# Optimization experiments

Hardware: AMD Instinct MI355X
Metric: run time of the kernel (lower is better)

## Reference

```python
import jax, jax.numpy as jnp
import numpy as np

MUL = 32          # channel multiplicity of node features (32x0e + 32x1o)
N_SPEC = 4        # one-hot species dim (node_attrs = 4x0e)
N_EMB = 8         # radial (bessel) embedding dim
HID = 8           # invariant_neurons
TP_W = 4 * MUL    # tp.weight_numel: 4 'uvu' paths, 32 weights each
INV_SQRT3 = 0.5773502691896258


def setup_inputs() -> dict:
    key = jax.random.key(0)
    ks = jax.random.split(key, 13)
    N, E = 50000, 800000
    node_features = jax.random.normal(ks[0], (N, 4 * MUL), jnp.float32)
    node_attrs = jax.random.uniform(ks[1], (N, N_SPEC), dtype=jnp.float32)
    edge_index = jax.random.randint(ks[2], (2, E), 0, N)
    edge_attrs = jax.random.normal(ks[3], (E, 4), jnp.float32)          # SH: [0e | 1o(3)]
    edge_embedding = jax.random.uniform(ks[4], (E, N_EMB), dtype=jnp.float32)
    # learned parameters
    W1_s = jax.random.normal(ks[5], (MUL, MUL), jnp.float32)            # linear_1 scalar block
    W1_v = jax.random.normal(ks[6], (MUL, MUL), jnp.float32)            # linear_1 vector block
    fc_w1 = jax.random.normal(ks[7], (N_EMB, HID), jnp.float32)         # radial MLP layer 1
    fc_w2 = jax.random.normal(ks[8], (HID, TP_W), jnp.float32)          # radial MLP -> tp weights
    W2_s = jax.random.normal(ks[9], (2 * MUL, MUL), jnp.float32)        # linear_2: 64x0e -> 32x0e
    W2_v = jax.random.normal(ks[10], (2 * MUL, MUL), jnp.float32)       # linear_2: 64x1o -> 32x1o
    Wsc_s = jax.random.normal(ks[11], (MUL, N_SPEC, MUL), jnp.float32)  # sc: 0e x 0e -> 0e (uvw)
    Wsc_v = jax.random.normal(ks[12], (MUL, N_SPEC, MUL), jnp.float32)  # sc: 1o x 0e -> 1o (uvw)
    return dict(node_features=node_features, node_attrs=node_attrs,
                edge_attrs=edge_attrs, edge_embedding=edge_embedding,
                W1_s=W1_s, W1_v=W1_v, fc_w1=fc_w1, fc_w2=fc_w2,
                W2_s=W2_s, W2_v=W2_v, Wsc_s=Wsc_s, Wsc_v=Wsc_v,
                edge_index=edge_index)


def reference(node_features, node_attrs, edge_attrs, edge_embedding,
              W1_s, W1_v, fc_w1, fc_w2, W2_s, W2_v, Wsc_s, Wsc_v, edge_index):
    N = node_features.shape[0]
    edge_src = edge_index[1]
    edge_dst = edge_index[0]

    # split node features into scalar (32x0e) and vector (32x1o) blocks
    s = node_features[:, :MUL]                       # [N, 32]
    v = node_features[:, MUL:].reshape(N, MUL, 3)    # [N, 32, 3]

    # --- self-connection: FullyConnectedTensorProduct(features, node_attrs) ---
    sc_norm = 1.0 / jnp.sqrt(jnp.float32(MUL * N_SPEC))
    sc_s = jnp.einsum('nu,na,uaw->nw', s, node_attrs, Wsc_s) * sc_norm
    sc_v = jnp.einsum('nui,na,uaw->nwi', v, node_attrs, Wsc_v) * sc_norm

    # --- linear_1 (per-irrep linear, fan-in normalized) ---
    l1 = 1.0 / jnp.sqrt(jnp.float32(MUL))
    s1 = (s @ W1_s) * l1                                   # [N, 32]
    v1 = jnp.einsum('nui,uw->nwi', v, W1_v) * l1           # [N, 32, 3]

    # --- radial MLP: edge_embedding -> per-edge tp weights (silu) ---
    h = jax.nn.silu((edge_embedding @ fc_w1) / jnp.sqrt(jnp.float32(N_EMB)))
    w = (h @ fc_w2) / jnp.sqrt(jnp.float32(HID))           # [E, 128]
    w0, w1, w2, w3 = w[:, :MUL], w[:, MUL:2*MUL], w[:, 2*MUL:3*MUL], w[:, 3*MUL:]

    # --- gather source-node features per edge ---
    ss = s1[edge_src]                                      # [E, 32]
    vv = v1[edge_src]                                      # [E, 32, 3]
    a0 = edge_attrs[:, 0]                                  # [E]    0e SH
    a1 = edge_attrs[:, 1:4]                                # [E, 3] 1o SH

    # --- 'uvu' CG tensor product (4 paths) with per-edge weights ---
    o_s0 = w0 * ss * a0[:, None]                                    # 0e x 0e -> 0e
    o_s1 = w3 * jnp.einsum('eui,ei->eu', vv, a1) * INV_SQRT3        # 1o x 1o -> 0e
    o_v0 = w1[:, :, None] * ss[:, :, None] * a1[:, None, :]        # 0e x 1o -> 1o
    o_v1 = w2[:, :, None] * vv * a0[:, None, None]                 # 1o x 0e -> 1o

    eS = jnp.concatenate([o_s0, o_s1], axis=1)             # [E, 64] (64x0e)
    eV = jnp.concatenate([o_v0, o_v1], axis=1)             # [E, 64, 3] (64x1o)

    # --- scatter-add to destination nodes ---
    S = jax.ops.segment_sum(eS, edge_dst, num_segments=N)  # [N, 64]
    V = jax.ops.segment_sum(eV, edge_dst, num_segments=N)  # [N, 64, 3]

    # --- linear_2 (64x0e+64x1o -> 32x0e+32x1o) ---
    l2 = 1.0 / jnp.sqrt(jnp.float32(2 * MUL))
    s_out = (S @ W2_s) * l2
    v_out = jnp.einsum('nui,uw->nwi', V, W2_v) * l2

    # --- residual self-connection ---
    s_out = s_out + sc_s
    v_out = v_out + sc_v
    return jnp.concatenate([s_out, v_out.reshape(N, MUL * 3)], axis=1)  # [N, 128]
```

## Files before the change

kernel.cpp:

```cpp
#include <hip/hip_runtime.h>
#include <math.h>


typedef float  v2f __attribute__((ext_vector_type(2)));
typedef float  v4f __attribute__((ext_vector_type(4)));

__device__ __forceinline__ unsigned short f2bf(float x) {
    unsigned u = __float_as_uint(x);
    u += 0x7FFFu + ((u >> 16) & 1u);
    return (unsigned short)(u >> 16);
}
__device__ __forceinline__ float bf2f(unsigned short h) {
    return __uint_as_float(((unsigned)h) << 16);
}

__global__ __launch_bounds__(256) void node_prep(
    const float* __restrict__ nf, const float* __restrict__ W1_s,
    const float* __restrict__ W1_v, const int* __restrict__ eidx,
    int* __restrict__ cnt, ushort* __restrict__ sv1, int N, int E)
{
    __shared__ float w1s[1024];
    __shared__ float w1v[1024];
    __shared__ float nrow[8][128];

    for (long long e = (long long)blockIdx.x * 256 + threadIdx.x; e < E;
         e += (long long)gridDim.x * 256)
        atomicAdd(cnt + eidx[(int)e], 1);

    int g = threadIdx.x >> 5;
    int w = threadIdx.x & 31;
    int n = blockIdx.x * 8 + g;

    for (int i = threadIdx.x; i < 1024; i += 256) {
        w1s[i] = W1_s[i];
        w1v[i] = W1_v[i];
    }
    if (n < N) {
        float4 q = *(const float4*)(nf + (size_t)n * 128 + w * 4);
        *(float4*)&nrow[g][w * 4] = q;
    }
    __syncthreads();
    if (n >= N) return;

    const float l1 = 0.17677669529663687f;
    const float* r = nrow[g];
    float ss = 0.f, vx = 0.f, vy = 0.f, vz = 0.f;
#pragma unroll 8
    for (int u = 0; u < 32; ++u) {
        float ws = w1s[u * 32 + w];
        float wv = w1v[u * 32 + w];
        ss += r[u] * ws;
        vx += r[32 + u * 3 + 0] * wv;
        vy += r[32 + u * 3 + 1] * wv;
        vz += r[32 + u * 3 + 2] * wv;
    }
    ushort4 o;
    o.x = f2bf(ss * l1); o.y = f2bf(vx * l1);
    o.z = f2bf(vy * l1); o.w = f2bf(vz * l1);
    *(ushort4*)(sv1 + (size_t)n * 128 + w * 4) = o;
}


__global__ __launch_bounds__(1024) void scan_a(
    const int* __restrict__ cnt, int* __restrict__ rs,
    int* __restrict__ bsum, int N)
{
    int i = blockIdx.x * 1024 + threadIdx.x;
    int lane = threadIdx.x & 63;
    int wid = threadIdx.x >> 6;
    int v = (i < N) ? cnt[i] : 0;
    int incl = v;
#pragma unroll
    for (int d = 1; d < 64; d <<= 1) {
        int t = __shfl_up(incl, d);
        if (lane >= d) incl += t;
    }
    __shared__ int wtot[16];
    __shared__ int woff[16];
    if (lane == 63) wtot[wid] = incl;
    __syncthreads();
    if (wid == 0) {
        int t = (lane < 16) ? wtot[lane] : 0;
        int s = t;
#pragma unroll
        for (int d = 1; d < 16; d <<= 1) {
            int q = __shfl_up(s, d);
            if (lane >= d) s += q;
        }
        if (lane < 16) woff[lane] = s - t;
        if (lane == 15) bsum[blockIdx.x] = s;
    }
    __syncthreads();
    if (i < N) rs[i] = woff[wid] + incl - v;
}

__global__ __launch_bounds__(64) void scan_b(
    const int* __restrict__ bsum, int* __restrict__ boff, int nb)
{
    int lane = threadIdx.x;
    int carry = 0;
    for (int base = 0; base < nb; base += 64) {
        int i = base + lane;
        int v = (i < nb) ? bsum[i] : 0;
        int s = v;
#pragma unroll
        for (int d = 1; d < 64; d <<= 1) {
            int t = __shfl_up(s, d);
            if (lane >= d) s += t;
        }
        if (i < nb) boff[i] = carry + s - v;
        carry += __shfl(s, 63);
    }
}

__global__ __launch_bounds__(256) void scatter_kernel(
    const int* __restrict__ eidx, int* __restrict__ rs,
    const int* __restrict__ boff, int* __restrict__ perm, int E)
{
    int e = blockIdx.x * 256 + threadIdx.x;
    if (e < E) {
        int d = eidx[e];
        int p = atomicAdd(rs + d, 1) + boff[d >> 10];
        perm[p] = e;
    }
}


__global__ __launch_bounds__(64) void reduce_kernel(
    const float* __restrict__ ea, const float* __restrict__ ee,
    const float* __restrict__ fc1, const float* __restrict__ fc2,
    const ushort* __restrict__ sv1, const int* __restrict__ eidx,
    const int* __restrict__ perm, const int* __restrict__ rs_end,
    const int* __restrict__ boff, const int* __restrict__ cnt,
    float* __restrict__ SV, int N, int E)
{
    __shared__ float rec[64][20];

    int l = threadIdx.x;
    int h = l >> 5;
    int u = l & 31;
    int n = blockIdx.x;

    const float rs8 = 0.35355339059327373f;
    const float inv_sqrt3 = 0.5773502691896258f;

    v2f f01[8], f23[8];
#pragma unroll
    for (int k = 0; k < 8; ++k) {
        f01[k].x = fc2[k * 128 + u];
        f01[k].y = fc2[k * 128 + 32 + u];
        f23[k].x = fc2[k * 128 + 64 + u];
        f23[k].y = fc2[k * 128 + 96 + u];
    }

    int count = cnt[n];
    int start = rs_end[n] + boff[n >> 10] - count;

    float aS0 = 0.f, aS1 = 0.f;
    float aV0x = 0.f, aV0y = 0.f, aV0z = 0.f;
    float aV1x = 0.f, aV1y = 0.f, aV1z = 0.f;

    for (int j0 = 0; j0 < count; j0 += 64) {
        int nk = count - j0; if (nk > 64) nk = 64;
        if (l < nk) {
            int e = perm[start + j0 + l];
            const float* eep = ee + (size_t)e * 8;
            v4f e0 = *(const v4f*)eep;
            v4f e1 = *(const v4f*)(eep + 4);
            float ev[8] = {e0.x, e0.y, e0.z, e0.w, e1.x, e1.y, e1.z, e1.w};
            float hh[8];
#pragma unroll
            for (int k = 0; k < 8; ++k) {
                float t = 0.f;
#pragma unroll
                for (int i = 0; i < 8; ++i) t += ev[i] * fc1[i * 8 + k];
                t *= rs8;
                hh[k] = t * __builtin_amdgcn_rcpf(1.f + __expf(-t)) * rs8;
            }
            float* rr = &rec[l][0];
            *(v4f*)rr       = (v4f){hh[0], hh[1], hh[2], hh[3]};
            *(v4f*)(rr + 4) = (v4f){hh[4], hh[5], hh[6], hh[7]};
            *(v4f*)(rr + 8) = *(const v4f*)(ea + (size_t)e * 4);
            rr[12] = __int_as_float(eidx[E + e]);
        }
        int pairs = (nk + 1) >> 1;
        int last = nk - 1;
        int s0 = __float_as_int(rec[h <= last ? h : last][12]);
        ushort4 q = *(const ushort4*)(sv1 + (size_t)s0 * 128 + u * 4);
        for (int jj = 0; jj < pairs; ++jj) {
            int slot = jj * 2 + h;
            int nslot = slot + 2 <= last ? slot + 2 : last;
            int sN = __float_as_int(rec[nslot][12]);
            ushort4 qn = *(const ushort4*)(sv1 + (size_t)sN * 128 + u * 4);

            float msk = (slot <= last) ? 1.f : 0.f;
            int slotc = slot <= last ? slot : last;
            const float* rr = &rec[slotc][0];
            v4f H0 = *(const v4f*)rr;
            v4f H1 = *(const v4f*)(rr + 4);
            v4f A  = *(const v4f*)(rr + 8);
            float ss = bf2f(q.x) * msk;
            float vx = bf2f(q.y), vy = bf2f(q.z), vz = bf2f(q.w);

            v2f w01 = H0.x * f01[0] + H0.y * f01[1] + H0.z * f01[2] + H0.w * f01[3]
                    + H1.x * f01[4] + H1.y * f01[5] + H1.z * f01[6] + H1.w * f01[7];
            v2f w23 = H0.x * f23[0] + H0.y * f23[1] + H0.z * f23[2] + H0.w * f23[3]
                    + H1.x * f23[4] + H1.y * f23[5] + H1.z * f23[6] + H1.w * f23[7];

            float dv = (vx * A.y + vy * A.z + vz * A.w) * msk;
            aS0 += w01.x * (ss * A.x);
            aS1 += w23.y * dv;
            float c1 = w01.y * ss;
            aV0x += c1 * A.y; aV0y += c1 * A.z; aV0z += c1 * A.w;
            float c2 = w23.x * A.x * msk;
            aV1x += c2 * vx; aV1y += c2 * vy; aV1z += c2 * vz;
            q = qn;
        }
    }

    aS0  += __shfl_xor(aS0, 32);
    aS1  += __shfl_xor(aS1, 32);
    aV0x += __shfl_xor(aV0x, 32);
    aV0y += __shfl_xor(aV0y, 32);
    aV0z += __shfl_xor(aV0z, 32);
    aV1x += __shfl_xor(aV1x, 32);
    aV1y += __shfl_xor(aV1y, 32);
    aV1z += __shfl_xor(aV1z, 32);

    if (h == 0) {
        float* o = SV + (size_t)n * 256 + u * 8;
        *(v4f*)o       = (v4f){aS0, aS1 * inv_sqrt3, aV0x, aV0y};
        *(v4f*)(o + 4) = (v4f){aV0z, aV1x, aV1y, aV1z};
    }
}


__global__ __launch_bounds__(256) void edge_kernel(
    const float* __restrict__ ea, const float* __restrict__ ee,
    const float* __restrict__ fc1, const float* __restrict__ fc2,
    const ushort* __restrict__ sv1, const int* __restrict__ eidx,
    float* __restrict__ SV, int E)
{
    long long tid = (long long)blockIdx.x * 256 + threadIdx.x;
    int e = (int)(tid >> 5);
    int u = (int)(tid & 31);
    if (e >= E) return;
    const float rs8 = 0.35355339059327373f;
    const float inv_sqrt3 = 0.5773502691896258f;
    float ev[8];
#pragma unroll
    for (int i = 0; i < 8; ++i) ev[i] = ee[(size_t)e * 8 + i];
    float h[8];
#pragma unroll
    for (int k = 0; k < 8; ++k) {
        float t = 0.f;
#pragma unroll
        for (int i = 0; i < 8; ++i) t += ev[i] * fc1[i * 8 + k];
        t *= rs8;
        h[k] = t / (1.f + expf(-t));
    }
    float w0 = 0.f, w1 = 0.f, w2 = 0.f, w3 = 0.f;
#pragma unroll
    for (int k = 0; k < 8; ++k) {
        const float* f2 = fc2 + k * 128;
        float hk = h[k];
        w0 += hk * f2[u];
        w1 += hk * f2[32 + u];
        w2 += hk * f2[64 + u];
        w3 += hk * f2[96 + u];
    }
    w0 *= rs8; w1 *= rs8; w2 *= rs8; w3 *= rs8;
    int dst = eidx[e];
    int src = eidx[E + e];
    float a0 = ea[(size_t)e * 4 + 0];
    float ax = ea[(size_t)e * 4 + 1];
    float ay = ea[(size_t)e * 4 + 2];
    float az = ea[(size_t)e * 4 + 3];
    ushort4 q = *(const ushort4*)(sv1 + (size_t)src * 128 + u * 4);
    float ss = bf2f(q.x), vx = bf2f(q.y), vy = bf2f(q.z), vz = bf2f(q.w);
    float dv = vx * ax + vy * ay + vz * az;
    float* o = SV + (size_t)dst * 256 + u * 8;
    atomicAdd(o + 0, w0 * ss * a0);
    atomicAdd(o + 1, w3 * dv * inv_sqrt3);
    float c1 = w1 * ss;
    atomicAdd(o + 2, c1 * ax);
    atomicAdd(o + 3, c1 * ay);
    atomicAdd(o + 4, c1 * az);
    float c2 = w2 * a0;
    atomicAdd(o + 5, c2 * vx);
    atomicAdd(o + 6, c2 * vy);
    atomicAdd(o + 7, c2 * vz);
}


__global__ __launch_bounds__(256) void node_final(
    const float* __restrict__ SV, const float* __restrict__ W2_s,
    const float* __restrict__ W2_v, const float* __restrict__ nf,
    const float* __restrict__ nattr, const float* __restrict__ Wsc_s,
    const float* __restrict__ Wsc_v, float* __restrict__ out, int N)
{
    __shared__ float wq[4096];
    __shared__ float wsp[4096];
    __shared__ float wvp[4096];
    __shared__ float svt[8][8][32];
    __shared__ float nrow[8][128];

    int g = threadIdx.x >> 5;
    int w = threadIdx.x & 31;

    for (int i = threadIdx.x; i < 1024; i += 256) {
        int uu = i >> 5, ww = i & 31;
        *(float4*)&wq[i * 4] = make_float4(W2_s[i], W2_s[i + 1024],
                                           W2_v[i], W2_v[i + 1024]);
        const float* ps = Wsc_s + (size_t)uu * 128 + ww;
        const float* pv = Wsc_v + (size_t)uu * 128 + ww;
        *(float4*)&wsp[i * 4] = make_float4(ps[0], ps[32], ps[64], ps[96]);
        *(float4*)&wvp[i * 4] = make_float4(pv[0], pv[32], pv[64], pv[96]);
    }
    __syncthreads();

    const float l2 = 0.125f;
    const float sc_norm = 0.08838834764831843f;

    for (int t = 0; t < 4; ++t) {
        int n = blockIdx.x * 32 + g * 4 + t;
        if (n >= N) continue;
        const float* svp = SV + (size_t)n * 256 + w * 8;
        float4 p0 = *(const float4*)svp;
        float4 p1 = *(const float4*)(svp + 4);
        svt[g][0][w] = p0.x; svt[g][1][w] = p0.y;
        svt[g][2][w] = p0.z; svt[g][3][w] = p0.w;
        svt[g][4][w] = p1.x; svt[g][5][w] = p1.y;
        svt[g][6][w] = p1.z; svt[g][7][w] = p1.w;
        float4 q = *(const float4*)(nf + (size_t)n * 128 + w * 4);
        *(float4*)&nrow[g][w * 4] = q;
        float at0 = nattr[(size_t)n * 4 + 0];
        float at1 = nattr[(size_t)n * 4 + 1];
        float at2 = nattr[(size_t)n * 4 + 2];
        float at3 = nattr[(size_t)n * 4 + 3];

        float sa = 0.f, va0 = 0.f, va1 = 0.f, va2 = 0.f;
        float scs = 0.f, scv0 = 0.f, scv1 = 0.f, scv2 = 0.f;
#pragma unroll
        for (int u = 0; u < 32; ++u) {
            float4 qw = *(const float4*)&wq[(u * 32 + w) * 4];
            sa  += svt[g][0][u] * qw.x + svt[g][1][u] * qw.y;
            va0 += svt[g][2][u] * qw.z + svt[g][5][u] * qw.w;
            va1 += svt[g][3][u] * qw.z + svt[g][6][u] * qw.w;
            va2 += svt[g][4][u] * qw.z + svt[g][7][u] * qw.w;
            float4 ps = *(const float4*)&wsp[(u * 32 + w) * 4];
            float4 pv = *(const float4*)&wvp[(u * 32 + w) * 4];
            float cs = at0 * ps.x + at1 * ps.y + at2 * ps.z + at3 * ps.w;
            float cv = at0 * pv.x + at1 * pv.y + at2 * pv.z + at3 * pv.w;
            scs  += nrow[g][u] * cs;
            scv0 += nrow[g][32 + u * 3 + 0] * cv;
            scv1 += nrow[g][32 + u * 3 + 1] * cv;
            scv2 += nrow[g][32 + u * 3 + 2] * cv;
        }
        float* orow = out + (size_t)n * 128;
        orow[w] = sa * l2 + scs * sc_norm;
        orow[32 + w * 3 + 0] = va0 * l2 + scv0 * sc_norm;
        orow[32 + w * 3 + 1] = va1 * l2 + scv1 * sc_norm;
        orow[32 + w * 3 + 2] = va2 * l2 + scv2 * sc_norm;
    }
}

extern "C" void kernel_launch(void* const* d_in, const int* in_sizes, int n_in,
                              void* d_out, int out_size, void* d_ws, size_t ws_size,
                              hipStream_t stream) {
    const float* nf    = (const float*)d_in[0];
    const float* nattr = (const float*)d_in[1];
    const float* ea    = (const float*)d_in[2];
    const float* ee    = (const float*)d_in[3];
    const float* W1_s  = (const float*)d_in[4];
    const float* W1_v  = (const float*)d_in[5];
    const float* fc1   = (const float*)d_in[6];
    const float* fc2   = (const float*)d_in[7];
    const float* W2_s  = (const float*)d_in[8];
    const float* W2_v  = (const float*)d_in[9];
    const float* Wsc_s = (const float*)d_in[10];
    const float* Wsc_v = (const float*)d_in[11];
    const int*   eidx  = (const int*)d_in[12];

    int N = in_sizes[0] / 128;
    int E = in_sizes[12] / 2;

    float* ws = (float*)d_ws;
    ushort* sv1 = (ushort*)ws;
    float* SV  = ws + (size_t)N * 64;
    int* cnt  = (int*)(SV + (size_t)N * 256);
    int* rs   = cnt + N;
    int* bsum = rs + N;
    int* boff = bsum + 64;
    int* perm = boff + 64;

    size_t needed = ((size_t)N * 320 + 2 * (size_t)N + 128 + (size_t)E) * 4;

    int nb_node = (N + 7) / 8;
    int nbE = (E + 255) / 256;
    int nb_final = (N + 31) / 32;

    if (ws_size >= needed) {
        hipMemsetAsync(cnt, 0, (size_t)N * sizeof(int), stream);
        node_prep<<<nb_node, 256, 0, stream>>>(nf, W1_s, W1_v, eidx, cnt, sv1, N, E);
        int nbS = (N + 1023) / 1024;
        scan_a<<<nbS, 1024, 0, stream>>>(cnt, rs, bsum, N);
        scan_b<<<1, 64, 0, stream>>>(bsum, boff, nbS);
        scatter_kernel<<<nbE, 256, 0, stream>>>(eidx, rs, boff, perm, E);
        reduce_kernel<<<N, 64, 0, stream>>>(ea, ee, fc1, fc2, sv1, eidx,
                                            perm, rs, boff, cnt, SV, N, E);
        node_final<<<nb_final, 256, 0, stream>>>(SV, W2_s, W2_v, nf, nattr,
                                                 Wsc_s, Wsc_v, (float*)d_out, N);
    } else {
        hipMemsetAsync(SV, 0, (size_t)N * 256 * sizeof(float), stream);
        node_prep<<<nb_node, 256, 0, stream>>>(nf, W1_s, W1_v, eidx, cnt, sv1, N, E);
        long long tot = (long long)E * 32;
        int nb_edge = (int)((tot + 255) / 256);
        edge_kernel<<<nb_edge, 256, 0, stream>>>(ea, ee, fc1, fc2, sv1, eidx, SV, E);
        node_final<<<nb_final, 256, 0, stream>>>(SV, W2_s, W2_v, nf, nattr,
                                                 Wsc_s, Wsc_v, (float*)d_out, N);
    }
}
```

Measured before the change: 251.8 us.

## Precompute radial MLP in scatter pass into sorted bf16 edge buffers

The scatter kernel now evaluates the radial MLP hidden layer per edge and writes the hidden values, edge attributes (both bf16) and source index directly into destination-sorted buffers. The reduce kernel no longer does random gathers through a permutation array or recomputes the MLP, and it reads contiguous records instead. The reduce kernel also packs two nodes per 128-thread block, and the intermediate SV buffer is stored in bf16 and read by a new node_final variant. This cuts gather traffic and SV bandwidth at the cost of extra bf16 rounding of hidden activations, edge attributes and aggregates.

```diff
diff --git a/kernel.cpp b/kernel.cpp
--- a/kernel.cpp
+++ b/kernel.cpp
@@ -13,6 +13,15 @@
 __device__ __forceinline__ float bf2f(unsigned short h) {
     return __uint_as_float(((unsigned)h) << 16);
 }
+__device__ __forceinline__ unsigned pack_bf(float lo, float hi) {
+    unsigned ul = __float_as_uint(lo);
+    ul = (ul + (0x7FFFu + ((ul >> 16) & 1u))) >> 16;
+    unsigned uh = __float_as_uint(hi);
+    uh = (uh + (0x7FFFu + ((uh >> 16) & 1u))) & 0xFFFF0000u;
+    return ul | uh;
+}
+__device__ __forceinline__ float bf_lo(unsigned p) { return __uint_as_float(p << 16); }
+__device__ __forceinline__ float bf_hi(unsigned p) { return __uint_as_float(p & 0xFFFF0000u); }
 
 __global__ __launch_bounds__(256) void node_prep(
     const float* __restrict__ nf, const float* __restrict__ W1_s,
@@ -113,35 +122,64 @@
     }
 }
 
-__global__ __launch_bounds__(256) void scatter_kernel(
-    const int* __restrict__ eidx, int* __restrict__ rs,
-    const int* __restrict__ boff, int* __restrict__ perm, int E)
+__global__ __launch_bounds__(256) void scatter_build(
+    const float* __restrict__ ea, const float* __restrict__ ee,
+    const float* __restrict__ fc1, const int* __restrict__ eidx,
+    int* __restrict__ rs, const int* __restrict__ boff,
+    ushort* __restrict__ hb, ushort* __restrict__ ab,
+    int* __restrict__ srcb, int E)
 {
     int e = blockIdx.x * 256 + threadIdx.x;
-    if (e < E) {
-        int d = eidx[e];
-        int p = atomicAdd(rs + d, 1) + boff[d >> 10];
-        perm[p] = e;
-    }
-}
-
-
-__global__ __launch_bounds__(64) void reduce_kernel(
-    const float* __restrict__ ea, const float* __restrict__ ee,
-    const float* __restrict__ fc1, const float* __restrict__ fc2,
-    const ushort* __restrict__ sv1, const int* __restrict__ eidx,
-    const int* __restrict__ perm, const int* __restrict__ rs_end,
+    if (e >= E) return;
+    const float rs8 = 0.35355339059327373f;
+
+    int d = eidx[e];
+    int p = atomicAdd(rs + d, 1) + boff[d >> 10];
+
+    const float* eep = ee + (size_t)e * 8;
+    v4f e0 = *(const v4f*)eep;
+    v4f e1 = *(const v4f*)(eep + 4);
+    float ev[8] = {e0.x, e0.y, e0.z, e0.w, e1.x, e1.y, e1.z, e1.w};
+    float hh[8];
+#pragma unroll
+    for (int k = 0; k < 8; ++k) {
+        float t = 0.f;
+#pragma unroll
+        for (int i = 0; i < 8; ++i) t += ev[i] * fc1[i * 8 + k];
+        t *= rs8;
+        hh[k] = t * __builtin_amdgcn_rcpf(1.f + __expf(-t)) * rs8;
+    }
+    uint4 hp;
+    hp.x = pack_bf(hh[0], hh[1]);
+    hp.y = pack_bf(hh[2], hh[3]);
+    hp.z = pack_bf(hh[4], hh[5]);
+    hp.w = pack_bf(hh[6], hh[7]);
+    *(uint4*)(hb + (size_t)p * 8) = hp;
+    v4f a = *(const v4f*)(ea + (size_t)e * 4);
+    uint2 ap;
+    ap.x = pack_bf(a.x, a.y);
+    ap.y = pack_bf(a.z, a.w);
+    *(uint2*)(ab + (size_t)p * 4) = ap;
+    srcb[p] = eidx[E + e];
+}
+
+
+__global__ __launch_bounds__(128) void reduce_kernel(
+    const float* __restrict__ fc2, const ushort* __restrict__ sv1,
+    const ushort* __restrict__ hb, const ushort* __restrict__ ab,
+    const int* __restrict__ srcb, const int* __restrict__ rs_end,
     const int* __restrict__ boff, const int* __restrict__ cnt,
-    float* __restrict__ SV, int N, int E)
-{
-    __shared__ float rec[64][20];
-
-    int l = threadIdx.x;
-    int h = l >> 5;
-    int u = l & 31;
-    int n = blockIdx.x;
-
-    const float rs8 = 0.35355339059327373f;
+    ushort* __restrict__ SVb, int N)
+{
+    __shared__ float rec[2][64][20];
+
+    int wv = threadIdx.x >> 6;
+    int l  = threadIdx.x & 63;
+    int h  = l >> 5;
+    int u  = l & 31;
+    int n = blockIdx.x * 2 + wv;
+    if (n >= N) return;
+
     const float inv_sqrt3 = 0.5773502691896258f;
 
     v2f f01[8], f23[8];
@@ -163,39 +201,29 @@
     for (int j0 = 0; j0 < count; j0 += 64) {
         int nk = count - j0; if (nk > 64) nk = 64;
         if (l < nk) {
-            int e = perm[start + j0 + l];
-            const float* eep = ee + (size_t)e * 8;
-            v4f e0 = *(const v4f*)eep;
-            v4f e1 = *(const v4f*)(eep + 4);
-            float ev[8] = {e0.x, e0.y, e0.z, e0.w, e1.x, e1.y, e1.z, e1.w};
-            float hh[8];
-#pragma unroll
-            for (int k = 0; k < 8; ++k) {
-                float t = 0.f;
-#pragma unroll
-                for (int i = 0; i < 8; ++i) t += ev[i] * fc1[i * 8 + k];
-                t *= rs8;
-                hh[k] = t * __builtin_amdgcn_rcpf(1.f + __expf(-t)) * rs8;
-            }
-            float* rr = &rec[l][0];
-            *(v4f*)rr       = (v4f){hh[0], hh[1], hh[2], hh[3]};
-            *(v4f*)(rr + 4) = (v4f){hh[4], hh[5], hh[6], hh[7]};
-            *(v4f*)(rr + 8) = *(const v4f*)(ea + (size_t)e * 4);
-            rr[12] = __int_as_float(eidx[E + e]);
+            size_t idx = (size_t)(start + j0 + l);
+            uint4 hq = *(const uint4*)(hb + idx * 8);
+            uint2 aq = *(const uint2*)(ab + idx * 4);
+            int s = srcb[idx];
+            float* rr = &rec[wv][l][0];
+            *(v4f*)rr       = (v4f){bf_lo(hq.x), bf_hi(hq.x), bf_lo(hq.y), bf_hi(hq.y)};
+            *(v4f*)(rr + 4) = (v4f){bf_lo(hq.z), bf_hi(hq.z), bf_lo(hq.w), bf_hi(hq.w)};
+            *(v4f*)(rr + 8) = (v4f){bf_lo(aq.x), bf_hi(aq.x), bf_lo(aq.y), bf_hi(aq.y)};
+            rr[12] = __int_as_float(s);
         }
         int pairs = (nk + 1) >> 1;
         int last = nk - 1;
-        int s0 = __float_as_int(rec[h <= last ? h : last][12]);
+        int s0 = __float_as_int(rec[wv][h <= last ? h : last][12]);
         ushort4 q = *(const ushort4*)(sv1 + (size_t)s0 * 128 + u * 4);
         for (int jj = 0; jj < pairs; ++jj) {
             int slot = jj * 2 + h;
             int nslot = slot + 2 <= last ? slot + 2 : last;
-            int sN = __float_as_int(rec[nslot][12]);
+            int sN = __float_as_int(rec[wv][nslot][12]);
             ushort4 qn = *(const ushort4*)(sv1 + (size_t)sN * 128 + u * 4);
 
             float msk = (slot <= last) ? 1.f : 0.f;
             int slotc = slot <= last ? slot : last;
-            const float* rr = &rec[slotc][0];
+            const float* rr = &rec[wv][slotc][0];
             v4f H0 = *(const v4f*)rr;
             v4f H1 = *(const v4f*)(rr + 4);
             v4f A  = *(const v4f*)(rr + 8);
@@ -228,9 +256,83 @@
     aV1z += __shfl_xor(aV1z, 32);
 
     if (h == 0) {
-        float* o = SV + (size_t)n * 256 + u * 8;
-        *(v4f*)o       = (v4f){aS0, aS1 * inv_sqrt3, aV0x, aV0y};
-        *(v4f*)(o + 4) = (v4f){aV0z, aV1x, aV1y, aV1z};
+        uint4 o;
+        o.x = pack_bf(aS0, aS1 * inv_sqrt3);
+        o.y = pack_bf(aV0x, aV0y);
+        o.z = pack_bf(aV0z, aV1x);
+        o.w = pack_bf(aV1y, aV1z);
+        *(uint4*)(SVb + (size_t)n * 256 + u * 8) = o;
+    }
+}
+
+
+__global__ __launch_bounds__(256) void node_final(
+    const ushort* __restrict__ SVb, const float* __restrict__ W2_s,
+    const float* __restrict__ W2_v, const float* __restrict__ nf,
+    const float* __restrict__ nattr, const float* __restrict__ Wsc_s,
+    const float* __restrict__ Wsc_v, float* __restrict__ out, int N)
+{
+    __shared__ float wq[4096];
+    __shared__ float wsp[4096];
+    __shared__ float wvp[4096];
+    __shared__ float svt[8][8][32];
+    __shared__ float nrow[8][128];
+
+    int g = threadIdx.x >> 5;
+    int w = threadIdx.x & 31;
+
+    for (int i = threadIdx.x; i < 1024; i += 256) {
+        int uu = i >> 5, ww = i & 31;
+        *(float4*)&wq[i * 4] = make_float4(W2_s[i], W2_s[i + 1024],
+                                           W2_v[i], W2_v[i + 1024]);
+        const float* ps = Wsc_s + (size_t)uu * 128 + ww;
+        const float* pv = Wsc_v + (size_t)uu * 128 + ww;
+        *(float4*)&wsp[i * 4] = make_float4(ps[0], ps[32], ps[64], ps[96]);
+        *(float4*)&wvp[i * 4] = make_float4(pv[0], pv[32], pv[64], pv[96]);
+    }
+    __syncthreads();
+
+    const float l2 = 0.125f;
+    const float sc_norm = 0.08838834764831843f;
+
+    for (int t = 0; t < 4; ++t) {
+        int n = blockIdx.x * 32 + g * 4 + t;
+        if (n >= N) continue;
+        uint4 p = *(const uint4*)(SVb + (size_t)n * 256 + w * 8);
+        svt[g][0][w] = bf_lo(p.x); svt[g][1][w] = bf_hi(p.x);
+        svt[g][2][w] = bf_lo(p.y); svt[g][3][w] = bf_hi(p.y);
+        svt[g][4][w] = bf_lo(p.z); svt[g][5][w] = bf_hi(p.z);
+        svt[g][6][w] = bf_lo(p.w); svt[g][7][w] = bf_hi(p.w);
+        float4 q = *(const float4*)(nf + (size_t)n * 128 + w * 4);
+        *(float4*)&nrow[g][w * 4] = q;
+        float at0 = nattr[(size_t)n * 4 + 0];
+        float at1 = nattr[(size_t)n * 4 + 1];
+        float at2 = nattr[(size_t)n * 4 + 2];
+        float at3 = nattr[(size_t)n * 4 + 3];
+
+        float sa = 0.f, va0 = 0.f, va1 = 0.f, va2 = 0.f;
+        float scs = 0.f, scv0 = 0.f, scv1 = 0.f, scv2 = 0.f;
+#pragma unroll
+        for (int u = 0; u < 32; ++u) {
+            float4 qw = *(const float4*)&wq[(u * 32 + w) * 4];
+            sa  += svt[g][0][u] * qw.x + svt[g][1][u] * qw.y;
+            va0 += svt[g][2][u] * qw.z + svt[g][5][u] * qw.w;
+            va1 += svt[g][3][u] * qw.z + svt[g][6][u] * qw.w;
+            va2 += svt[g][4][u] * qw.z + svt[g][7][u] * qw.w;
+            float4 ps = *(const float4*)&wsp[(u * 32 + w) * 4];
+            float4 pv = *(const float4*)&wvp[(u * 32 + w) * 4];
+            float cs = at0 * ps.x + at1 * ps.y + at2 * ps.z + at3 * ps.w;
+            float cv = at0 * pv.x + at1 * pv.y + at2 * pv.z + at3 * pv.w;
+            scs  += nrow[g][u] * cs;
+            scv0 += nrow[g][32 + u * 3 + 0] * cv;
+            scv1 += nrow[g][32 + u * 3 + 1] * cv;
+            scv2 += nrow[g][32 + u * 3 + 2] * cv;
+        }
+        float* orow = out + (size_t)n * 128;
+        orow[w] = sa * l2 + scs * sc_norm;
+        orow[32 + w * 3 + 0] = va0 * l2 + scv0 * sc_norm;
+        orow[32 + w * 3 + 1] = va1 * l2 + scv1 * sc_norm;
+        orow[32 + w * 3 + 2] = va2 * l2 + scv2 * sc_norm;
     }
 }
 
@@ -292,8 +394,7 @@
     atomicAdd(o + 7, c2 * vz);
 }
 
-
-__global__ __launch_bounds__(256) void node_final(
+__global__ __launch_bounds__(256) void node_final_f32(
     const float* __restrict__ SV, const float* __restrict__ W2_s,
     const float* __restrict__ W2_v, const float* __restrict__ nf,
     const float* __restrict__ nattr, const float* __restrict__ Wsc_s,
@@ -387,14 +488,16 @@
 
     float* ws = (float*)d_ws;
     ushort* sv1 = (ushort*)ws;
-    float* SV  = ws + (size_t)N * 64;
-    int* cnt  = (int*)(SV + (size_t)N * 256);
+    ushort* SVb = (ushort*)(ws + (size_t)N * 64);
+    ushort* hb  = (ushort*)(ws + (size_t)N * 192);
+    ushort* ab  = (ushort*)(ws + (size_t)N * 192 + (size_t)E * 4);
+    int* srcb = (int*)(ws + (size_t)N * 192 + (size_t)E * 6);
+    int* cnt  = srcb + E;
     int* rs   = cnt + N;
     int* bsum = rs + N;
     int* boff = bsum + 64;
-    int* perm = boff + 64;
-
-    size_t needed = ((size_t)N * 320 + 2 * (size_t)N + 128 + (size_t)E) * 4;
+
+    size_t needed = ((size_t)N * 194 + (size_t)E * 7 + 128) * 4;
 
     int nb_node = (N + 7) / 8;
     int nbE = (E + 255) / 256;
@@ -406,18 +509,22 @@
         int nbS = (N + 1023) / 1024;
         scan_a<<<nbS, 1024, 0, stream>>>(cnt, rs, bsum, N);
         scan_b<<<1, 64, 0, stream>>>(bsum, boff, nbS);
-        scatter_kernel<<<nbE, 256, 0, stream>>>(eidx, rs, boff, perm, E);
-        reduce_kernel<<<N, 64, 0, stream>>>(ea, ee, fc1, fc2, sv1, eidx,
-                                            perm, rs, boff, cnt, SV, N, E);
-        node_final<<<nb_final, 256, 0, stream>>>(SV, W2_s, W2_v, nf, nattr,
+        scatter_build<<<nbE, 256, 0, stream>>>(ea, ee, fc1, eidx, rs, boff,
+                                               hb, ab, srcb, E);
+        int nbR = (N + 1) / 2;
+        reduce_kernel<<<nbR, 128, 0, stream>>>(fc2, sv1, hb, ab, srcb,
+                                               rs, boff, cnt, SVb, N);
+        node_final<<<nb_final, 256, 0, stream>>>(SVb, W2_s, W2_v, nf, nattr,
                                                  Wsc_s, Wsc_v, (float*)d_out, N);
     } else {
-        hipMemsetAsync(SV, 0, (size_t)N * 256 * sizeof(float), stream);
-        node_prep<<<nb_node, 256, 0, stream>>>(nf, W1_s, W1_v, eidx, cnt, sv1, N, E);
+        float* SVf = ws + (size_t)N * 64;
+        int* cnt_f = (int*)(SVf + (size_t)N * 256);
+        hipMemsetAsync(SVf, 0, (size_t)N * 256 * sizeof(float), stream);
+        node_prep<<<nb_node, 256, 0, stream>>>(nf, W1_s, W1_v, eidx, cnt_f, sv1, N, E);
         long long tot = (long long)E * 32;
         int nb_edge = (int)((tot + 255) / 256);
-        edge_kernel<<<nb_edge, 256, 0, stream>>>(ea, ee, fc1, fc2, sv1, eidx, SV, E);
-        node_final<<<nb_final, 256, 0, stream>>>(SV, W2_s, W2_v, nf, nattr,
-                                                 Wsc_s, Wsc_v, (float*)d_out, N);
-    }
-}
+        edge_kernel<<<nb_edge, 256, 0, stream>>>(ea, ee, fc1, fc2, sv1, eidx, SVf, E);
+        node_final_f32<<<nb_final, 256, 0, stream>>>(SVf, W2_s, W2_v, nf, nattr,
+                                                     Wsc_s, Wsc_v, (float*)d_out, N);
+    }
+}
```

Measured after the change: 237.9 us. 5.6% less time.
